# Performance work log

Hardware: AMD Instinct MI355X
Metric: run time of the kernel (lower is better)

## Reference

```python
import jax, jax.numpy as jnp
import numpy as np

HID = 128      # hidden_dim
CDIM = 128     # c_dim
NBLK = 5       # n_blocks
RESO = 32      # grid_resolution
G = RESO ** 3  # number of voxels
B, T = 2, 100000


def setup_inputs() -> dict:
    key = jax.random.key(0)
    ks = jax.random.split(key, 8)
    return {
        "points": jax.random.normal(ks[0], (B, T, 3), jnp.float32),
        "index": jax.random.randint(ks[1], (B, 1, T), 0, G, dtype=jnp.int64),
        # fc_pos: Linear(3, 2*HID)
        "fc_pos_w": jax.random.normal(ks[2], (3, 2 * HID), jnp.float32) * 0.1,
        "fc_pos_b": jnp.zeros((2 * HID,), jnp.float32),
        # ResnetBlockFC(2*HID, HID) x NBLK: fc_0 (2H->H), fc_1 (H->H), shortcut (2H->H, no bias)
        "fc0_w": jax.random.normal(ks[3], (NBLK, 2 * HID, HID), jnp.float32) * 0.05,
        "fc0_b": jnp.zeros((NBLK, HID), jnp.float32),
        "fc1_w": jax.random.normal(ks[4], (NBLK, HID, HID), jnp.float32) * 0.05,
        "fc1_b": jnp.zeros((NBLK, HID), jnp.float32),
        "sc_w": jax.random.normal(ks[5], (NBLK, 2 * HID, HID), jnp.float32) * 0.05,
        # fc_c: Linear(HID, CDIM)
        "fc_c_w": jax.random.normal(ks[6], (HID, CDIM), jnp.float32) * 0.05,
        "fc_c_b": jnp.zeros((CDIM,), jnp.float32),
    }


def _resnet_block(x, w0, b0, w1, b1, ws):
    # ResnetBlockFC: net = fc_0(relu(x)); dx = fc_1(relu(net)); out = shortcut(x) + dx
    net = jnp.maximum(x, 0.0) @ w0 + b0
    dx = jnp.maximum(net, 0.0) @ w1 + b1
    return x @ ws + dx


def reference(points, index, fc_pos_w, fc_pos_b, fc0_w, fc0_b, fc1_w, fc1_b, sc_w, fc_c_w, fc_c_b):
    idx = index[:, 0, :]  # [B, T]

    def pool_local(net):
        # scatter_max over voxels, then gather back per point
        seg = jax.vmap(lambda c_b, i_b: jax.ops.segment_max(c_b, i_b, num_segments=G))(net, idx)  # [B,G,H]
        return jnp.take_along_axis(seg, idx[:, :, None], axis=1)  # [B,T,H]; every gathered voxel is non-empty

    net = points @ fc_pos_w + fc_pos_b          # [B,T,2H]
    net = _resnet_block(net, fc0_w[0], fc0_b[0], fc1_w[0], fc1_b[0], sc_w[0])  # [B,T,H]
    for i in range(1, NBLK):
        pooled = pool_local(net)
        net = jnp.concatenate([net, pooled], axis=2)  # [B,T,2H]
        net = _resnet_block(net, fc0_w[i], fc0_b[i], fc1_w[i], fc1_b[i], sc_w[i])

    c = net @ fc_c_w + fc_c_b  # [B,T,CDIM]

    # generate_grid_features: scatter_mean into the 32^3 grid (zeros for empty voxels)
    sums = jax.vmap(lambda c_b, i_b: jax.ops.segment_sum(c_b, i_b, num_segments=G))(c, idx)  # [B,G,CDIM]
    cnts = jax.vmap(lambda i_b: jax.ops.segment_sum(jnp.ones((T,), c.dtype), i_b, num_segments=G))(idx)  # [B,G]
    cnts = cnts[:, :, None]
    mean = jnp.where(cnts > 0, sums / jnp.maximum(cnts, 1.0), 0.0)
    fea_grid = jnp.transpose(mean, (0, 2, 1)).reshape(B, CDIM, RESO, RESO, RESO)
    return fea_grid
```

## Files before the change

### kernel.cpp

```cpp
#include <hip/hip_runtime.h>

#define T_PTS 100000
#define NB 2
#define GCELLS 32768
#define NCELL (NB * GCELLS)
#define HID 128
#define MBLK 64
#define RBPB 1563
#define GRID_RB (NB * RBPB)

typedef __attribute__((ext_vector_type(8))) short bf16x8;
typedef __attribute__((ext_vector_type(4))) float f32x4;

#define MFMA16 __builtin_amdgcn_mfma_f32_16x16x32_bf16

__device__ __forceinline__ unsigned short bf16rne(float f) {
  unsigned u = __float_as_uint(f);
  return (unsigned short)((u + 0x7FFFu + ((u >> 16) & 1u)) >> 16);
}

template <int MODE>
__global__ __launch_bounds__(256, 4) void resblock_mfma(
    const float* __restrict__ src, const float* __restrict__ posw,
    const float* __restrict__ posb, const float* __restrict__ cell,
    const int* __restrict__ idx, const unsigned short* __restrict__ w0p,
    const float* __restrict__ b0, const unsigned short* __restrict__ w1p,
    const float* __restrict__ b1, const unsigned short* __restrict__ swp,
    float* __restrict__ net_out) {
  __shared__ unsigned short lds[16384];
  const int tid = threadIdx.x;
  const int lane = tid & 63;
  const int wc = tid >> 6;
  const int b = blockIdx.x / RBPB;
  const int t0 = (blockIdx.x % RBPB) * MBLK;
  const int valid = (T_PTS - t0 < MBLK) ? (T_PTS - t0) : MBLK;

  f32x4 accy[4][2], acco[4][2];
#pragma unroll
  for (int i = 0; i < 4; ++i)
#pragma unroll
    for (int j = 0; j < 2; ++j) {
      f32x4 z = {0.f, 0.f, 0.f, 0.f};
      accy[i][j] = z;
      acco[i][j] = z;
    }

  auto stage = [&](int ks) {
    const int slot = ks & 1;
    const int pt = tid >> 2;
    const int kc = (tid & 3) << 3;
    float xv[8];
    if (MODE == 0) {
      float p0 = 0.f, p1 = 0.f, p2 = 0.f;
      if (pt < valid) {
        const float* pp = src + ((long)b * T_PTS + t0 + pt) * 3;
        p0 = pp[0]; p1 = pp[1]; p2 = pp[2];
      }
      const int kb = ks * 32 + kc;
#pragma unroll
      for (int i = 0; i < 8; i += 4) {
        float4 wa = *(const float4*)(posw + kb + i);
        float4 wb = *(const float4*)(posw + 256 + kb + i);
        float4 wcc = *(const float4*)(posw + 512 + kb + i);
        float4 bb = *(const float4*)(posb + kb + i);
        xv[i + 0] = fmaf(p0, wa.x, fmaf(p1, wb.x, fmaf(p2, wcc.x, bb.x)));
        xv[i + 1] = fmaf(p0, wa.y, fmaf(p1, wb.y, fmaf(p2, wcc.y, bb.y)));
        xv[i + 2] = fmaf(p0, wa.z, fmaf(p1, wb.z, fmaf(p2, wcc.z, bb.z)));
        xv[i + 3] = fmaf(p0, wa.w, fmaf(p1, wb.w, fmaf(p2, wcc.w, bb.w)));
      }
    } else {
      if (pt < valid) {
        const float* rp;
        if (ks < 4) {
          rp = src + ((long)b * T_PTS + t0 + pt) * HID + ks * 32 + kc;
        } else {
          const int g = idx[(long)b * T_PTS + t0 + pt];
          rp = cell + ((long)b * GCELLS + g) * HID + (ks - 4) * 32 + kc;
        }
        float4 v0 = *(const float4*)(rp);
        float4 v1 = *(const float4*)(rp + 4);
        xv[0] = v0.x; xv[1] = v0.y; xv[2] = v0.z; xv[3] = v0.w;
        xv[4] = v1.x; xv[5] = v1.y; xv[6] = v1.z; xv[7] = v1.w;
      } else {
#pragma unroll
        for (int i = 0; i < 8; ++i) xv[i] = 0.f;
      }
    }
    bf16x8 vh, vl, vrh, vrl;
#pragma unroll
    for (int i = 0; i < 8; ++i) {
      float x = xv[i];
      unsigned short h = bf16rne(x);
      float hf = __uint_as_float(((unsigned)h) << 16);
      unsigned short lo = bf16rne(x - hf);
      bool pos = x > 0.f;
      vh[i] = (short)h;
      vl[i] = (short)lo;
      vrh[i] = pos ? (short)h : (short)0;
      vrl[i] = pos ? (short)lo : (short)0;
    }
    const int l = (kc >> 3) * 16 + (pt & 15);
    const int base = slot * 8192 + (pt >> 4) * 512 + l * 8;
    *(bf16x8*)(lds + base) = vh;
    *(bf16x8*)(lds + base + 2048) = vl;
    *(bf16x8*)(lds + base + 4096) = vrh;
    *(bf16x8*)(lds + base + 6144) = vrl;
  };

  stage(0);
  __syncthreads();

#pragma unroll 1
  for (int ks = 0; ks < 8; ++ks) {
    if (ks < 7) stage(ks + 1);
    const int slot = ks & 1;
    {
      bf16x8 bh[2], bl[2];
#pragma unroll
      for (int nt = 0; nt < 2; ++nt) {
        const int fi = (ks * 8 + wc * 2 + nt) * 512 + lane * 8;
        bh[nt] = *(const bf16x8*)(w0p + fi);
        bl[nt] = *(const bf16x8*)(w0p + 32768 + fi);
      }
#pragma unroll
      for (int mt = 0; mt < 4; ++mt) {
        const int ab = slot * 8192 + mt * 512 + lane * 8;
        bf16x8 arh = *(const bf16x8*)(lds + ab + 4096);
        bf16x8 arl = *(const bf16x8*)(lds + ab + 6144);
#pragma unroll
        for (int nt = 0; nt < 2; ++nt) {
          accy[mt][nt] = MFMA16(arh, bh[nt], accy[mt][nt], 0, 0, 0);
          accy[mt][nt] = MFMA16(arh, bl[nt], accy[mt][nt], 0, 0, 0);
          accy[mt][nt] = MFMA16(arl, bh[nt], accy[mt][nt], 0, 0, 0);
        }
      }
    }
    {
      bf16x8 bh[2], bl[2];
#pragma unroll
      for (int nt = 0; nt < 2; ++nt) {
        const int fi = (ks * 8 + wc * 2 + nt) * 512 + lane * 8;
        bh[nt] = *(const bf16x8*)(swp + fi);
        bl[nt] = *(const bf16x8*)(swp + 32768 + fi);
      }
#pragma unroll
      for (int mt = 0; mt < 4; ++mt) {
        const int ab = slot * 8192 + mt * 512 + lane * 8;
        bf16x8 axh = *(const bf16x8*)(lds + ab);
        bf16x8 axl = *(const bf16x8*)(lds + ab + 2048);
#pragma unroll
        for (int nt = 0; nt < 2; ++nt) {
          acco[mt][nt] = MFMA16(axh, bh[nt], acco[mt][nt], 0, 0, 0);
          acco[mt][nt] = MFMA16(axh, bl[nt], acco[mt][nt], 0, 0, 0);
          acco[mt][nt] = MFMA16(axl, bh[nt], acco[mt][nt], 0, 0, 0);
        }
      }
    }
    __syncthreads();
  }

  {
    float b0v[2];
#pragma unroll
    for (int nt = 0; nt < 2; ++nt)
      b0v[nt] = b0[wc * 32 + nt * 16 + (lane & 15)];
#pragma unroll
    for (int mt = 0; mt < 4; ++mt) {
#pragma unroll
      for (int nt = 0; nt < 2; ++nt) {
        const int c = wc * 32 + nt * 16 + (lane & 15);
        const int k2 = c >> 5;
        const int j = c & 7;
        const int lahi = ((c & 31) >> 3) * 16;
#pragma unroll
        for (int r = 0; r < 4; ++r) {
          float h = fmaxf(accy[mt][nt][r] + b0v[nt], 0.f);
          unsigned short hh = bf16rne(h);
          float hf = __uint_as_float(((unsigned)hh) << 16);
          unsigned short hl = bf16rne(h - hf);
          int la = lahi + (lane >> 4) * 4 + r;
          la ^= (la >> 3) & 7;
          const int off = ((k2 * 4 + mt) * 64 + la) * 8 + j;
          lds[off] = hh;
          lds[off + 8192] = hl;
        }
      }
    }
  }
  __syncthreads();

  {
    const int lar = lane ^ ((lane >> 3) & 7);
#pragma unroll
    for (int k2 = 0; k2 < 4; ++k2) {
      bf16x8 bh[2], bl[2];
#pragma unroll
      for (int nt = 0; nt < 2; ++nt) {
        const int fi = (k2 * 8 + wc * 2 + nt) * 512 + lane * 8;
        bh[nt] = *(const bf16x8*)(w1p + fi);
        bl[nt] = *(const bf16x8*)(w1p + 16384 + fi);
      }
#pragma unroll
      for (int mt = 0; mt < 4; ++mt) {
        const int ab = ((k2 * 4 + mt) * 64 + lar) * 8;
        bf16x8 ah = *(const bf16x8*)(lds + ab);
        bf16x8 al = *(const bf16x8*)(lds + ab + 8192);
#pragma unroll
        for (int nt = 0; nt < 2; ++nt) {
          acco[mt][nt] = MFMA16(ah, bh[nt], acco[mt][nt], 0, 0, 0);
          acco[mt][nt] = MFMA16(ah, bl[nt], acco[mt][nt], 0, 0, 0);
          acco[mt][nt] = MFMA16(al, bh[nt], acco[mt][nt], 0, 0, 0);
        }
      }
    }
  }

  {
    float b1v[2];
#pragma unroll
    for (int nt = 0; nt < 2; ++nt)
      b1v[nt] = b1[wc * 32 + nt * 16 + (lane & 15)];
#pragma unroll
    for (int mt = 0; mt < 4; ++mt) {
#pragma unroll
      for (int r = 0; r < 4; ++r) {
        const int row = mt * 16 + (lane >> 4) * 4 + r;
        if (row < valid) {
          float* op = net_out + ((long)b * T_PTS + t0 + row) * HID;
          op[wc * 32 + (lane & 15)] = acco[mt][0][r] + b1v[0];
          op[wc * 32 + 16 + (lane & 15)] = acco[mt][1][r] + b1v[1];
        }
      }
    }
  }
}

__global__ __launch_bounds__(256, 4) void final_mfma(
    float* __restrict__ net, const unsigned short* __restrict__ wcp,
    const float* __restrict__ bc) {
  __shared__ unsigned short lds[8192];
  const int tid = threadIdx.x;
  const int lane = tid & 63;
  const int wc = tid >> 6;
  const int b = blockIdx.x / RBPB;
  const int t0 = (blockIdx.x % RBPB) * MBLK;
  const int valid = (T_PTS - t0 < MBLK) ? (T_PTS - t0) : MBLK;

  f32x4 acc[4][2];
#pragma unroll
  for (int i = 0; i < 4; ++i)
#pragma unroll
    for (int j = 0; j < 2; ++j) {
      f32x4 z = {0.f, 0.f, 0.f, 0.f};
      acc[i][j] = z;
    }

  auto stage = [&](int ks) {
    const int slot = ks & 1;
    const int pt = tid >> 2;
    const int kc = (tid & 3) << 3;
    float xv[8];
    if (pt < valid) {
      const float* rp = net + ((long)b * T_PTS + t0 + pt) * HID + ks * 32 + kc;
      float4 v0 = *(const float4*)(rp);
      float4 v1 = *(const float4*)(rp + 4);
      xv[0] = v0.x; xv[1] = v0.y; xv[2] = v0.z; xv[3] = v0.w;
      xv[4] = v1.x; xv[5] = v1.y; xv[6] = v1.z; xv[7] = v1.w;
    } else {
#pragma unroll
      for (int i = 0; i < 8; ++i) xv[i] = 0.f;
    }
    bf16x8 vh, vl;
#pragma unroll
    for (int i = 0; i < 8; ++i) {
      float x = xv[i];
      unsigned short h = bf16rne(x);
      float hf = __uint_as_float(((unsigned)h) << 16);
      unsigned short lo = bf16rne(x - hf);
      vh[i] = (short)h;
      vl[i] = (short)lo;
    }
    const int l = (kc >> 3) * 16 + (pt & 15);
    const int base = slot * 4096 + (pt >> 4) * 512 + l * 8;
    *(bf16x8*)(lds + base) = vh;
    *(bf16x8*)(lds + base + 2048) = vl;
  };

  stage(0);
  __syncthreads();
#pragma unroll 1
  for (int ks = 0; ks < 4; ++ks) {
    if (ks < 3) stage(ks + 1);
    const int slot = ks & 1;
    bf16x8 bh[2], bl[2];
#pragma unroll
    for (int nt = 0; nt < 2; ++nt) {
      const int fi = (ks * 8 + wc * 2 + nt) * 512 + lane * 8;
      bh[nt] = *(const bf16x8*)(wcp + fi);
      bl[nt] = *(const bf16x8*)(wcp + 16384 + fi);
    }
#pragma unroll
    for (int mt = 0; mt < 4; ++mt) {
      const int ab = slot * 4096 + mt * 512 + lane * 8;
      bf16x8 ah = *(const bf16x8*)(lds + ab);
      bf16x8 al = *(const bf16x8*)(lds + ab + 2048);
#pragma unroll
      for (int nt = 0; nt < 2; ++nt) {
        acc[mt][nt] = MFMA16(ah, bh[nt], acc[mt][nt], 0, 0, 0);
        acc[mt][nt] = MFMA16(ah, bl[nt], acc[mt][nt], 0, 0, 0);
        acc[mt][nt] = MFMA16(al, bh[nt], acc[mt][nt], 0, 0, 0);
      }
    }
    __syncthreads();
  }

  float bcv[2];
#pragma unroll
  for (int nt = 0; nt < 2; ++nt)
    bcv[nt] = bc[wc * 32 + nt * 16 + (lane & 15)];
#pragma unroll
  for (int mt = 0; mt < 4; ++mt) {
#pragma unroll
    for (int r = 0; r < 4; ++r) {
      const int row = mt * 16 + (lane >> 4) * 4 + r;
      if (row < valid) {
        float* op = net + ((long)b * T_PTS + t0 + row) * HID;
        op[wc * 32 + (lane & 15)] = acc[mt][0][r] + bcv[0];
        op[wc * 32 + 16 + (lane & 15)] = acc[mt][1][r] + bcv[1];
      }
    }
  }
}

__global__ void pack_weights(const float* __restrict__ fc0,
                             const float* __restrict__ fc1,
                             const float* __restrict__ sc,
                             const float* __restrict__ fcc,
                             unsigned short* __restrict__ w0p,
                             unsigned short* __restrict__ w1p,
                             unsigned short* __restrict__ swp,
                             unsigned short* __restrict__ wcp) {
  int gid = blockIdx.x * 256 + threadIdx.x;
  const float* src;
  unsigned short* dst;
  int K, e;
  if (gid < 163840) { src = fc0; dst = w0p; K = 256; e = gid; }
  else if (gid < 327680) { src = sc; dst = swp; K = 256; e = gid - 163840; }
  else if (gid < 409600) { src = fc1; dst = w1p; K = 128; e = gid - 327680; }
  else if (gid < 425984) { src = fcc; dst = wcp; K = 128; e = gid - 409600; }
  else return;
  const int mat = e / (K * 128);
  const int r = e - mat * K * 128;
  const int k = r >> 7, n = r & 127;
  const float x = src[e];
  const unsigned short hi = bf16rne(x);
  const float hf = __uint_as_float(((unsigned)hi) << 16);
  const unsigned short lo = bf16rne(x - hf);
  const int ks = k >> 5, lg = (k >> 3) & 3, j = k & 7;
  const int l = lg * 16 + (n & 15), nt = n >> 4;
  unsigned short* mb = dst + (long)mat * K * 256;
  const int off = ((ks * 8 + nt) * 64 + l) * 8 + j;
  mb[off] = hi;
  mb[off + K * 128] = lo;
}

__global__ void zero_i32(int* __restrict__ p, int n) {
  const int i = blockIdx.x * 256 + threadIdx.x;
  if (i < n) p[i] = 0;
}

__global__ void count_csr(const int* __restrict__ idx, int* __restrict__ curs) {
  const int gid = blockIdx.x * 256 + threadIdx.x;
  if (gid >= NB * T_PTS) return;
  const int b = gid / T_PTS;
  atomicAdd(&curs[b * GCELLS + idx[gid]], 1);
}

__global__ __launch_bounds__(1024) void scan_csr(const int* __restrict__ cnt,
                                                 int* __restrict__ offsets) {
  __shared__ int part[1024];
  const int t = threadIdx.x;
  const int base = t * (NCELL / 1024);
  int s = 0;
  for (int i = 0; i < NCELL / 1024; ++i) s += cnt[base + i];
  part[t] = s;
  __syncthreads();
  for (int d = 1; d < 1024; d <<= 1) {
    int v = (t >= d) ? part[t - d] : 0;
    __syncthreads();
    part[t] += v;
    __syncthreads();
  }
  int run = (t == 0) ? 0 : part[t - 1];
  for (int i = 0; i < NCELL / 1024; ++i) {
    offsets[base + i] = run;
    run += cnt[base + i];
  }
  if (t == 1023) offsets[NCELL] = run;
}

__global__ void scatter_csr(const int* __restrict__ idx,
                            const int* __restrict__ offsets,
                            int* __restrict__ curs, int* __restrict__ perm) {
  const int gid = blockIdx.x * 256 + threadIdx.x;
  if (gid >= NB * T_PTS) return;
  const int b = gid / T_PTS;
  const int cellk = b * GCELLS + idx[gid];
  const int slot = offsets[cellk] + atomicAdd(&curs[cellk], 1);
  perm[slot] = gid;
}

__global__ __launch_bounds__(256) void pool_csr(const float* __restrict__ net,
                                                const int* __restrict__ perm,
                                                const int* __restrict__ offsets,
                                                float* __restrict__ cellf) {
  const int cellk = blockIdx.x * 4 + (threadIdx.x >> 6);
  const int lane = threadIdx.x & 63;
  const int s0 = offsets[cellk], s1 = offsets[cellk + 1];
  if (s0 >= s1) return;
  float2 m = {-3.402823466e38f, -3.402823466e38f};
  for (int j = s0; j < s1; ++j) {
    const long row = perm[j];
    float2 v = *(const float2*)(net + row * HID + lane * 2);
    m.x = fmaxf(m.x, v.x);
    m.y = fmaxf(m.y, v.y);
  }
  *(float2*)(cellf + (long)cellk * HID + lane * 2) = m;
}

__global__ __launch_bounds__(256) void cellsum_csr(
    const float* __restrict__ c, const int* __restrict__ perm,
    const int* __restrict__ offsets, float* __restrict__ sums) {
  const int cellk = blockIdx.x * 4 + (threadIdx.x >> 6);
  const int lane = threadIdx.x & 63;
  const int s0 = offsets[cellk], s1 = offsets[cellk + 1];
  if (s0 >= s1) return;
  float2 m = {0.f, 0.f};
  for (int j = s0; j < s1; ++j) {
    const long row = perm[j];
    float2 v = *(const float2*)(c + row * HID + lane * 2);
    m.x += v.x;
    m.y += v.y;
  }
  *(float2*)(sums + (long)cellk * HID + lane * 2) = m;
}

__global__ void mean_kernel(const float* __restrict__ sums,
                            const int* __restrict__ offsets,
                            float* __restrict__ out) {
  const long gid = (long)blockIdx.x * 256 + threadIdx.x;
  if (gid >= (long)NB * HID * GCELLS) return;
  const int g = (int)(gid % GCELLS);
  const int c = (int)((gid / GCELLS) % HID);
  const int b = (int)(gid / ((long)HID * GCELLS));
  const int cellk = b * GCELLS + g;
  const int cnt = offsets[cellk + 1] - offsets[cellk];
  out[gid] = cnt > 0 ? sums[(long)cellk * HID + c] / (float)cnt : 0.f;
}

extern "C" void kernel_launch(void* const* d_in, const int* in_sizes, int n_in,
                              void* d_out, int out_size, void* d_ws,
                              size_t ws_size, hipStream_t stream) {
  const float* points = (const float*)d_in[0];
  const int* idx = (const int*)d_in[1];
  const float* fc_pos_w = (const float*)d_in[2];
  const float* fc_pos_b = (const float*)d_in[3];
  const float* fc0_w = (const float*)d_in[4];
  const float* fc0_b = (const float*)d_in[5];
  const float* fc1_w = (const float*)d_in[6];
  const float* fc1_b = (const float*)d_in[7];
  const float* sc_w = (const float*)d_in[8];
  const float* fc_c_w = (const float*)d_in[9];
  const float* fc_c_b = (const float*)d_in[10];
  float* out = (float*)d_out;

  const long NET_BYTES = (long)NB * T_PTS * HID * 4;
  const long CELL_BYTES = (long)NB * GCELLS * HID * 4;
  float* net = (float*)d_ws;
  float* cellf = (float*)((char*)d_ws + NET_BYTES);
  float* sums = cellf;
  int* offsets = (int*)((char*)d_ws + NET_BYTES + CELL_BYTES);

  unsigned short* packs = (unsigned short*)d_out;
  unsigned short* w0p = packs;
  unsigned short* swp = packs + 327680;
  unsigned short* w1p = packs + 655360;
  unsigned short* wcp = packs + 819200;
  int* curs = (int*)((char*)d_out + (2l << 20));
  int* perm = (int*)((char*)d_out + (3l << 20));

  const int GRID_PTS = (NB * T_PTS + 255) / 256;
  const int GRID_ZERO = (NCELL + 255) / 256;
  const int GRID_CELL = NCELL / 4;
  const int GRID_MEAN = NB * HID * GCELLS / 256;

  pack_weights<<<1664, 256, 0, stream>>>(fc0_w, fc1_w, sc_w, fc_c_w, w0p, w1p,
                                         swp, wcp);

  zero_i32<<<GRID_ZERO, 256, 0, stream>>>(curs, NCELL);
  count_csr<<<GRID_PTS, 256, 0, stream>>>(idx, curs);
  scan_csr<<<1, 1024, 0, stream>>>(curs, offsets);
  zero_i32<<<GRID_ZERO, 256, 0, stream>>>(curs, NCELL);
  scatter_csr<<<GRID_PTS, 256, 0, stream>>>(idx, offsets, curs, perm);

  resblock_mfma<0><<<GRID_RB, 256, 0, stream>>>(
      points, fc_pos_w, fc_pos_b, nullptr, nullptr, w0p, fc0_b, w1p, fc1_b,
      swp, net);

  for (int i = 1; i < 5; ++i) {
    pool_csr<<<GRID_CELL, 256, 0, stream>>>(net, perm, offsets, cellf);
    resblock_mfma<1><<<GRID_RB, 256, 0, stream>>>(
        net, nullptr, nullptr, cellf, idx, w0p + (long)i * 65536,
        fc0_b + i * HID, w1p + (long)i * 32768, fc1_b + i * HID,
        swp + (long)i * 65536, net);
  }

  final_mfma<<<GRID_RB, 256, 0, stream>>>(net, wcp, fc_c_b);
  cellsum_csr<<<GRID_CELL, 256, 0, stream>>>(net, perm, offsets, sums);
  mean_kernel<<<GRID_MEAN, 256, 0, stream>>>(sums, offsets, out);
}
```

Measured before the change: 784.1 us.

## Store activations as packed bf16 hi/lo pairs to skip per-stage split conversion

The intermediate net buffer and pooled cell features now hold each value as a packed 32-bit bf16 hi/lo pair, computed once by the producer. The MFMA staging code only has to permute bytes into the LDS layout instead of redoing the float-to-bf16 split on every load. Global loads for the next k-slice are issued before the MFMA work and written to LDS after it, so load latency can overlap compute. LDS stores and reads use an XOR swizzle to reduce bank conflicts. Pooling picks the max by comparing the reconstructed hi+lo value, which keeps precision close to the float path at the cost of slightly more ALU per element.

```diff
diff --git a/kernel.cpp b/kernel.cpp
--- a/kernel.cpp
+++ b/kernel.cpp
@@ -18,15 +18,23 @@
   unsigned u = __float_as_uint(f);
   return (unsigned short)((u + 0x7FFFu + ((u >> 16) & 1u)) >> 16);
 }
+__device__ __forceinline__ unsigned packhl(float f) {
+  unsigned short h = bf16rne(f);
+  float hf = __uint_as_float(((unsigned)h) << 16);
+  unsigned short l = bf16rne(f - hf);
+  return (((unsigned)h) << 16) | (unsigned)l;
+}
+
+union U8 { bf16x8 v; unsigned u[4]; };
 
 template <int MODE>
 __global__ __launch_bounds__(256, 4) void resblock_mfma(
-    const float* __restrict__ src, const float* __restrict__ posw,
-    const float* __restrict__ posb, const float* __restrict__ cell,
+    const void* __restrict__ srcv, const float* __restrict__ posw,
+    const float* __restrict__ posb, const unsigned* __restrict__ cell,
     const int* __restrict__ idx, const unsigned short* __restrict__ w0p,
     const float* __restrict__ b0, const unsigned short* __restrict__ w1p,
     const float* __restrict__ b1, const unsigned short* __restrict__ swp,
-    float* __restrict__ net_out) {
+    unsigned* __restrict__ net_out) {
   __shared__ unsigned short lds[16384];
   const int tid = threadIdx.x;
   const int lane = tid & 63;
@@ -35,85 +43,102 @@
   const int t0 = (blockIdx.x % RBPB) * MBLK;
   const int valid = (T_PTS - t0 < MBLK) ? (T_PTS - t0) : MBLK;
 
-  f32x4 accy[4][2], acco[4][2];
-#pragma unroll
-  for (int i = 0; i < 4; ++i)
-#pragma unroll
-    for (int j = 0; j < 2; ++j) {
-      f32x4 z = {0.f, 0.f, 0.f, 0.f};
-      accy[i][j] = z;
-      acco[i][j] = z;
-    }
-
-  auto stage = [&](int ks) {
-    const int slot = ks & 1;
-    const int pt = tid >> 2;
-    const int kc = (tid & 3) << 3;
-    float xv[8];
-    if (MODE == 0) {
-      float p0 = 0.f, p1 = 0.f, p2 = 0.f;
-      if (pt < valid) {
-        const float* pp = src + ((long)b * T_PTS + t0 + pt) * 3;
-        p0 = pp[0]; p1 = pp[1]; p2 = pp[2];
-      }
+  const int pt = tid >> 2;
+  const int kc = (tid & 3) << 3;
+  const int lstore = ((tid & 3) * 16 + (pt & 15)) ^ (tid & 3);
+  const int sbase0 = (pt >> 4) * 512 + lstore * 8;
+  const bool pv = (pt < valid);
+
+  const unsigned* nrow = nullptr;
+  const unsigned* crow = nullptr;
+  float pp0 = 0.f, pp1 = 0.f, pp2 = 0.f;
+  if (MODE == 1) {
+    if (pv) {
+      const long prow = (long)b * T_PTS + t0 + pt;
+      nrow = (const unsigned*)srcv + prow * HID;
+      crow = cell + ((long)b * GCELLS + idx[prow]) * HID;
+    }
+  } else {
+    if (pv) {
+      const float* ppp = (const float*)srcv + ((long)b * T_PTS + t0 + pt) * 3;
+      pp0 = ppp[0]; pp1 = ppp[1]; pp2 = ppp[2];
+    }
+  }
+
+  auto load_x = [&](int ks, unsigned* w) {
+    if (MODE == 1) {
+      if (pv) {
+        const unsigned* rp = (ks < 4) ? (nrow + ks * 32 + kc)
+                                      : (crow + (ks - 4) * 32 + kc);
+        uint4 a = *(const uint4*)rp;
+        uint4 c = *(const uint4*)(rp + 4);
+        w[0] = a.x; w[1] = a.y; w[2] = a.z; w[3] = a.w;
+        w[4] = c.x; w[5] = c.y; w[6] = c.z; w[7] = c.w;
+      } else {
+#pragma unroll
+        for (int i = 0; i < 8; ++i) w[i] = 0u;
+      }
+    } else {
       const int kb = ks * 32 + kc;
+      float xv[8];
 #pragma unroll
       for (int i = 0; i < 8; i += 4) {
         float4 wa = *(const float4*)(posw + kb + i);
         float4 wb = *(const float4*)(posw + 256 + kb + i);
         float4 wcc = *(const float4*)(posw + 512 + kb + i);
         float4 bb = *(const float4*)(posb + kb + i);
-        xv[i + 0] = fmaf(p0, wa.x, fmaf(p1, wb.x, fmaf(p2, wcc.x, bb.x)));
-        xv[i + 1] = fmaf(p0, wa.y, fmaf(p1, wb.y, fmaf(p2, wcc.y, bb.y)));
-        xv[i + 2] = fmaf(p0, wa.z, fmaf(p1, wb.z, fmaf(p2, wcc.z, bb.z)));
-        xv[i + 3] = fmaf(p0, wa.w, fmaf(p1, wb.w, fmaf(p2, wcc.w, bb.w)));
-      }
-    } else {
-      if (pt < valid) {
-        const float* rp;
-        if (ks < 4) {
-          rp = src + ((long)b * T_PTS + t0 + pt) * HID + ks * 32 + kc;
-        } else {
-          const int g = idx[(long)b * T_PTS + t0 + pt];
-          rp = cell + ((long)b * GCELLS + g) * HID + (ks - 4) * 32 + kc;
-        }
-        float4 v0 = *(const float4*)(rp);
-        float4 v1 = *(const float4*)(rp + 4);
-        xv[0] = v0.x; xv[1] = v0.y; xv[2] = v0.z; xv[3] = v0.w;
-        xv[4] = v1.x; xv[5] = v1.y; xv[6] = v1.z; xv[7] = v1.w;
-      } else {
-#pragma unroll
-        for (int i = 0; i < 8; ++i) xv[i] = 0.f;
-      }
-    }
-    bf16x8 vh, vl, vrh, vrl;
-#pragma unroll
-    for (int i = 0; i < 8; ++i) {
-      float x = xv[i];
-      unsigned short h = bf16rne(x);
-      float hf = __uint_as_float(((unsigned)h) << 16);
-      unsigned short lo = bf16rne(x - hf);
-      bool pos = x > 0.f;
-      vh[i] = (short)h;
-      vl[i] = (short)lo;
-      vrh[i] = pos ? (short)h : (short)0;
-      vrl[i] = pos ? (short)lo : (short)0;
-    }
-    const int l = (kc >> 3) * 16 + (pt & 15);
-    const int base = slot * 8192 + (pt >> 4) * 512 + l * 8;
-    *(bf16x8*)(lds + base) = vh;
-    *(bf16x8*)(lds + base + 2048) = vl;
-    *(bf16x8*)(lds + base + 4096) = vrh;
-    *(bf16x8*)(lds + base + 6144) = vrl;
+        xv[i + 0] = fmaf(pp0, wa.x, fmaf(pp1, wb.x, fmaf(pp2, wcc.x, bb.x)));
+        xv[i + 1] = fmaf(pp0, wa.y, fmaf(pp1, wb.y, fmaf(pp2, wcc.y, bb.y)));
+        xv[i + 2] = fmaf(pp0, wa.z, fmaf(pp1, wb.z, fmaf(pp2, wcc.z, bb.z)));
+        xv[i + 3] = fmaf(pp0, wa.w, fmaf(pp1, wb.w, fmaf(pp2, wcc.w, bb.w)));
+      }
+#pragma unroll
+      for (int i = 0; i < 8; ++i) w[i] = pv ? packhl(xv[i]) : 0u;
+    }
   };
 
-  stage(0);
+  auto store_x = [&](int ks, const unsigned* w) {
+    const int base = ((ks & 1) << 13) + sbase0;
+    U8 vh, vl, vrh, vrl;
+#pragma unroll
+    for (int p = 0; p < 4; ++p) {
+      const unsigned w0 = w[2 * p], w1 = w[2 * p + 1];
+      const unsigned r0 = ((int)w0 < 0) ? 0u : w0;
+      const unsigned r1 = ((int)w1 < 0) ? 0u : w1;
+      vh.u[p] = __builtin_amdgcn_perm(w1, w0, 0x07060302u);
+      vl.u[p] = __builtin_amdgcn_perm(w1, w0, 0x05040100u);
+      vrh.u[p] = __builtin_amdgcn_perm(r1, r0, 0x07060302u);
+      vrl.u[p] = __builtin_amdgcn_perm(r1, r0, 0x05040100u);
+    }
+    *(bf16x8*)(lds + base) = vh.v;
+    *(bf16x8*)(lds + base + 2048) = vl.v;
+    *(bf16x8*)(lds + base + 4096) = vrh.v;
+    *(bf16x8*)(lds + base + 6144) = vrl.v;
+  };
+
+  f32x4 accy[4][2], acco[4][2];
+#pragma unroll
+  for (int i = 0; i < 4; ++i)
+#pragma unroll
+    for (int j = 0; j < 2; ++j) {
+      f32x4 z = {0.f, 0.f, 0.f, 0.f};
+      accy[i][j] = z;
+      acco[i][j] = z;
+    }
+
+  {
+    unsigned w[8];
+    load_x(0, w);
+    store_x(0, w);
+  }
   __syncthreads();
 
+  const int lar = lane ^ ((lane >> 4) & 3);
 #pragma unroll 1
   for (int ks = 0; ks < 8; ++ks) {
-    if (ks < 7) stage(ks + 1);
-    const int slot = ks & 1;
+    unsigned nxt[8];
+    if (ks < 7) load_x(ks + 1, nxt);
+    const int sb = (ks & 1) << 13;
     {
       bf16x8 bh[2], bl[2];
 #pragma unroll
@@ -124,7 +149,7 @@
       }
 #pragma unroll
       for (int mt = 0; mt < 4; ++mt) {
-        const int ab = slot * 8192 + mt * 512 + lane * 8;
+        const int ab = sb + mt * 512 + lar * 8;
         bf16x8 arh = *(const bf16x8*)(lds + ab + 4096);
         bf16x8 arl = *(const bf16x8*)(lds + ab + 6144);
 #pragma unroll
@@ -145,7 +170,7 @@
       }
 #pragma unroll
       for (int mt = 0; mt < 4; ++mt) {
-        const int ab = slot * 8192 + mt * 512 + lane * 8;
+        const int ab = sb + mt * 512 + lar * 8;
         bf16x8 axh = *(const bf16x8*)(lds + ab);
         bf16x8 axl = *(const bf16x8*)(lds + ab + 2048);
 #pragma unroll
@@ -156,6 +181,7 @@
         }
       }
     }
+    if (ks < 7) store_x(ks + 1, nxt);
     __syncthreads();
   }
 
@@ -180,9 +206,9 @@
           unsigned short hl = bf16rne(h - hf);
           int la = lahi + (lane >> 4) * 4 + r;
           la ^= (la >> 3) & 7;
-          const int off = ((k2 * 4 + mt) * 64 + la) * 8 + j;
-          lds[off] = hh;
-          lds[off + 8192] = hl;
+          const int o = ((k2 * 4 + mt) * 64 + la) * 8 + j;
+          lds[o] = hh;
+          lds[o + 8192] = hl;
         }
       }
     }
@@ -190,7 +216,7 @@
   __syncthreads();
 
   {
-    const int lar = lane ^ ((lane >> 3) & 7);
+    const int lar2 = lane ^ ((lane >> 3) & 7);
 #pragma unroll
     for (int k2 = 0; k2 < 4; ++k2) {
       bf16x8 bh[2], bl[2];
@@ -202,7 +228,7 @@
       }
 #pragma unroll
       for (int mt = 0; mt < 4; ++mt) {
-        const int ab = ((k2 * 4 + mt) * 64 + lar) * 8;
+        const int ab = ((k2 * 4 + mt) * 64 + lar2) * 8;
         bf16x8 ah = *(const bf16x8*)(lds + ab);
         bf16x8 al = *(const bf16x8*)(lds + ab + 8192);
 #pragma unroll
@@ -226,9 +252,9 @@
       for (int r = 0; r < 4; ++r) {
         const int row = mt * 16 + (lane >> 4) * 4 + r;
         if (row < valid) {
-          float* op = net_out + ((long)b * T_PTS + t0 + row) * HID;
-          op[wc * 32 + (lane & 15)] = acco[mt][0][r] + b1v[0];
-          op[wc * 32 + 16 + (lane & 15)] = acco[mt][1][r] + b1v[1];
+          unsigned* op = net_out + ((long)b * T_PTS + t0 + row) * HID;
+          op[wc * 32 + (lane & 15)] = packhl(acco[mt][0][r] + b1v[0]);
+          op[wc * 32 + 16 + (lane & 15)] = packhl(acco[mt][1][r] + b1v[1]);
         }
       }
     }
@@ -236,7 +262,7 @@
 }
 
 __global__ __launch_bounds__(256, 4) void final_mfma(
-    float* __restrict__ net, const unsigned short* __restrict__ wcp,
+    unsigned* __restrict__ net, const unsigned short* __restrict__ wcp,
     const float* __restrict__ bc) {
   __shared__ unsigned short lds[8192];
   const int tid = threadIdx.x;
@@ -246,6 +272,38 @@
   const int t0 = (blockIdx.x % RBPB) * MBLK;
   const int valid = (T_PTS - t0 < MBLK) ? (T_PTS - t0) : MBLK;
 
+  const int pt = tid >> 2;
+  const int kc = (tid & 3) << 3;
+  const int lstore = ((tid & 3) * 16 + (pt & 15)) ^ (tid & 3);
+  const int sbase0 = (pt >> 4) * 512 + lstore * 8;
+  const bool pv = (pt < valid);
+  const unsigned* nrow = pv ? net + ((long)b * T_PTS + t0 + pt) * HID : nullptr;
+
+  auto load_x = [&](int ks, unsigned* w) {
+    if (pv) {
+      const unsigned* rp = nrow + ks * 32 + kc;
+      uint4 a = *(const uint4*)rp;
+      uint4 c = *(const uint4*)(rp + 4);
+      w[0] = a.x; w[1] = a.y; w[2] = a.z; w[3] = a.w;
+      w[4] = c.x; w[5] = c.y; w[6] = c.z; w[7] = c.w;
+    } else {
+#pragma unroll
+      for (int i = 0; i < 8; ++i) w[i] = 0u;
+    }
+  };
+  auto store_x = [&](int ks, const unsigned* w) {
+    const int base = ((ks & 1) << 12) + sbase0;
+    U8 vh, vl;
+#pragma unroll
+    for (int p = 0; p < 4; ++p) {
+      const unsigned w0 = w[2 * p], w1 = w[2 * p + 1];
+      vh.u[p] = __builtin_amdgcn_perm(w1, w0, 0x07060302u);
+      vl.u[p] = __builtin_amdgcn_perm(w1, w0, 0x05040100u);
+    }
+    *(bf16x8*)(lds + base) = vh.v;
+    *(bf16x8*)(lds + base + 2048) = vl.v;
+  };
+
   f32x4 acc[4][2];
 #pragma unroll
   for (int i = 0; i < 4; ++i)
@@ -255,43 +313,19 @@
       acc[i][j] = z;
     }
 
-  auto stage = [&](int ks) {
-    const int slot = ks & 1;
-    const int pt = tid >> 2;
-    const int kc = (tid & 3) << 3;
-    float xv[8];
-    if (pt < valid) {
-      const float* rp = net + ((long)b * T_PTS + t0 + pt) * HID + ks * 32 + kc;
-      float4 v0 = *(const float4*)(rp);
-      float4 v1 = *(const float4*)(rp + 4);
-      xv[0] = v0.x; xv[1] = v0.y; xv[2] = v0.z; xv[3] = v0.w;
-      xv[4] = v1.x; xv[5] = v1.y; xv[6] = v1.z; xv[7] = v1.w;
-    } else {
-#pragma unroll
-      for (int i = 0; i < 8; ++i) xv[i] = 0.f;
-    }
-    bf16x8 vh, vl;
-#pragma unroll
-    for (int i = 0; i < 8; ++i) {
-      float x = xv[i];
-      unsigned short h = bf16rne(x);
-      float hf = __uint_as_float(((unsigned)h) << 16);
-      unsigned short lo = bf16rne(x - hf);
-      vh[i] = (short)h;
-      vl[i] = (short)lo;
-    }
-    const int l = (kc >> 3) * 16 + (pt & 15);
-    const int base = slot * 4096 + (pt >> 4) * 512 + l * 8;
-    *(bf16x8*)(lds + base) = vh;
-    *(bf16x8*)(lds + base + 2048) = vl;
-  };
-
-  stage(0);
+  {
+    unsigned w[8];
+    load_x(0, w);
+    store_x(0, w);
+  }
   __syncthreads();
+
+  const int lar = lane ^ ((lane >> 4) & 3);
 #pragma unroll 1
   for (int ks = 0; ks < 4; ++ks) {
-    if (ks < 3) stage(ks + 1);
-    const int slot = ks & 1;
+    unsigned nxt[8];
+    if (ks < 3) load_x(ks + 1, nxt);
+    const int sb = (ks & 1) << 12;
     bf16x8 bh[2], bl[2];
 #pragma unroll
     for (int nt = 0; nt < 2; ++nt) {
@@ -301,7 +335,7 @@
     }
 #pragma unroll
     for (int mt = 0; mt < 4; ++mt) {
-      const int ab = slot * 4096 + mt * 512 + lane * 8;
+      const int ab = sb + mt * 512 + lar * 8;
       bf16x8 ah = *(const bf16x8*)(lds + ab);
       bf16x8 al = *(const bf16x8*)(lds + ab + 2048);
 #pragma unroll
@@ -311,9 +345,11 @@
         acc[mt][nt] = MFMA16(al, bh[nt], acc[mt][nt], 0, 0, 0);
       }
     }
+    if (ks < 3) store_x(ks + 1, nxt);
     __syncthreads();
   }
 
+  float* fout = (float*)net;
   float bcv[2];
 #pragma unroll
   for (int nt = 0; nt < 2; ++nt)
@@ -324,7 +360,7 @@
     for (int r = 0; r < 4; ++r) {
       const int row = mt * 16 + (lane >> 4) * 4 + r;
       if (row < valid) {
-        float* op = net + ((long)b * T_PTS + t0 + row) * HID;
+        float* op = fout + ((long)b * T_PTS + t0 + row) * HID;
         op[wc * 32 + (lane & 15)] = acc[mt][0][r] + bcv[0];
         op[wc * 32 + 16 + (lane & 15)] = acc[mt][1][r] + bcv[1];
       }
@@ -410,22 +446,26 @@
   perm[slot] = gid;
 }
 
-__global__ __launch_bounds__(256) void pool_csr(const float* __restrict__ net,
+__global__ __launch_bounds__(256) void pool_csr(const unsigned* __restrict__ net,
                                                 const int* __restrict__ perm,
                                                 const int* __restrict__ offsets,
-                                                float* __restrict__ cellf) {
+                                                unsigned* __restrict__ cellf) {
   const int cellk = blockIdx.x * 4 + (threadIdx.x >> 6);
   const int lane = threadIdx.x & 63;
   const int s0 = offsets[cellk], s1 = offsets[cellk + 1];
   if (s0 >= s1) return;
-  float2 m = {-3.402823466e38f, -3.402823466e38f};
+  float m0 = -3.402823466e38f, m1 = -3.402823466e38f;
+  unsigned b0 = 0u, b1 = 0u;
   for (int j = s0; j < s1; ++j) {
     const long row = perm[j];
-    float2 v = *(const float2*)(net + row * HID + lane * 2);
-    m.x = fmaxf(m.x, v.x);
-    m.y = fmaxf(m.y, v.y);
-  }
-  *(float2*)(cellf + (long)cellk * HID + lane * 2) = m;
+    uint2 w = *(const uint2*)(net + row * HID + lane * 2);
+    float v0 = __uint_as_float(w.x & 0xFFFF0000u) + __uint_as_float(w.x << 16);
+    float v1 = __uint_as_float(w.y & 0xFFFF0000u) + __uint_as_float(w.y << 16);
+    if (v0 > m0) { m0 = v0; b0 = w.x; }
+    if (v1 > m1) { m1 = v1; b1 = w.y; }
+  }
+  uint2 o; o.x = b0; o.y = b1;
+  *(uint2*)(cellf + (long)cellk * HID + lane * 2) = o;
 }
 
 __global__ __launch_bounds__(256) void cellsum_csr(
@@ -476,9 +516,9 @@
 
   const long NET_BYTES = (long)NB * T_PTS * HID * 4;
   const long CELL_BYTES = (long)NB * GCELLS * HID * 4;
-  float* net = (float*)d_ws;
-  float* cellf = (float*)((char*)d_ws + NET_BYTES);
-  float* sums = cellf;
+  unsigned* net = (unsigned*)d_ws;
+  unsigned* cellf = (unsigned*)((char*)d_ws + NET_BYTES);
+  float* sums = (float*)cellf;
   int* offsets = (int*)((char*)d_ws + NET_BYTES + CELL_BYTES);
 
   unsigned short* packs = (unsigned short*)d_out;
@@ -516,6 +556,7 @@
   }
 
   final_mfma<<<GRID_RB, 256, 0, stream>>>(net, wcp, fc_c_b);
-  cellsum_csr<<<GRID_CELL, 256, 0, stream>>>(net, perm, offsets, sums);
+  cellsum_csr<<<GRID_CELL, 256, 0, stream>>>((const float*)net, perm, offsets,
+                                             sums);
   mean_kernel<<<GRID_MEAN, 256, 0, stream>>>(sums, offsets, out);
 }
```

After: 786.8 us. About the same (+0.3%).
